# Kernel tuning notes

Measured on AMD Instinct MI355X. Metric: run time of the kernel, lower is better.

## Reference

```python
import jax, jax.numpy as jnp
import numpy as np

N = 4096          # batch size / number of points
D_DATA = 1024     # data feature dim
D_LATENT = 64     # latent dim
REG_LAMBDA = 0.5


def _pdist(x):
    """Pairwise Euclidean distance matrix [N, N] via the gram trick.

    Equivalent to norm(x[None, :, :] - x[:, None, :], axis=-1) but avoids the
    N x N x D intermediate. Safe sqrt so the (zero) diagonal has zero gradient.
    """
    sq = jnp.sum(x * x, axis=-1)                      # [N]
    g = x @ x.T                                       # [N, N] gram
    d2 = jnp.maximum(sq[:, None] + sq[None, :] - 2.0 * g, 0.0)
    pos = d2 > 0
    d = jnp.sqrt(jnp.where(pos, d2, 1.0))
    return jnp.where(pos, d, 0.0)


def _mst_edges(dist):
    """Edges (i, j) of the minimum spanning tree of the complete graph with
    edge weights dist[i, j] (0d persistent homology death edges).
    Prim's algorithm, vectorized per step via lax.scan. Returns [N-1, 2] int32.
    """
    n = dist.shape[0]
    in_tree = jnp.zeros(n, dtype=bool).at[0].set(True)
    min_dist = dist[0]                                # best distance to tree
    min_src = jnp.zeros(n, dtype=jnp.int32)           # tree node achieving it

    def step(carry, _):
        in_tree, min_dist, min_src = carry
        masked = jnp.where(in_tree, jnp.inf, min_dist)
        j = jnp.argmin(masked).astype(jnp.int32)
        edge = jnp.stack([min_src[j], j])
        in_tree = in_tree.at[j].set(True)
        dj = dist[j]
        upd = dj < min_dist
        min_dist = jnp.where(upd, dj, min_dist)
        min_src = jnp.where(upd, j, min_src)
        return (in_tree, min_dist, min_src), edge

    _, edges = jax.lax.scan(step, (in_tree, min_dist, min_src), None, length=n - 1)
    return edges  # [N-1, 2]


def _gather(dist, edges):
    return dist[edges[:, 0], edges[:, 1]]  # [N-1]


def setup_inputs() -> dict:
    key = jax.random.key(0)
    k1, k2, k3 = jax.random.split(key, 3)
    return {
        "y_true": jax.random.normal(k1, (N, D_DATA), dtype=jnp.float32),
        "latent": jax.random.normal(k2, (N, D_LATENT), dtype=jnp.float32),
        "y_pred": jax.random.normal(k3, (N, D_DATA), dtype=jnp.float32),
        "latent_norm": jnp.array(1.0, dtype=jnp.float32),
    }


def reference(y_true, latent, y_pred, latent_norm):
    # keras MSE: mean over last axis -> per-sample vector [N]
    ae_loss = jnp.mean((y_true - y_pred) ** 2, axis=-1)

    data_distances = _pdist(y_true)
    data_distances = data_distances / jnp.max(data_distances)
    latent_distances = _pdist(latent) / latent_norm

    e_data = _mst_edges(jax.lax.stop_gradient(data_distances))
    data_loss = jnp.mean((_gather(data_distances, e_data)
                          - _gather(latent_distances, e_data)) ** 2)

    e_lat = _mst_edges(jax.lax.stop_gradient(latent_distances))
    latent_loss = jnp.mean((_gather(data_distances, e_lat)
                            - _gather(latent_distances, e_lat)) ** 2)

    topo_loss = data_loss + latent_loss
    return ae_loss + REG_LAMBDA * topo_loss  # [N] (scalar topo broadcast)
```

## Files before the change

### kernel.cpp

```cpp
#include <hip/hip_runtime.h>
#include <math.h>

#define N_PTS 4096
#define DD 1024
#define DL 64
#define NEDGE (N_PTS - 1)
#define B_ROUNDS 12
#define NT 32

typedef __attribute__((ext_vector_type(8))) short short8;
typedef __attribute__((ext_vector_type(4))) float floatx4;
typedef __attribute__((ext_vector_type(4))) unsigned short ushortx4;

__device__ __forceinline__ unsigned short f2bf(float f) {
  unsigned u = __float_as_uint(f);
  u = u + 0x7FFFu + ((u >> 16) & 1u);
  return (unsigned short)(u >> 16);
}

__global__ __launch_bounds__(256) void ae_sq_kernel(const float* __restrict__ yt,
                                                    const float* __restrict__ yp,
                                                    float* __restrict__ out,
                                                    float* __restrict__ sqD,
                                                    unsigned short* __restrict__ Xb) {
  int row = blockIdx.x, tid = threadIdx.x;
  const float4* a = (const float4*)(yt + (size_t)row * DD);
  const float4* b = (const float4*)(yp + (size_t)row * DD);
  float4 va = a[tid], vb = b[tid];
  ushortx4 o = {f2bf(va.x), f2bf(va.y), f2bf(va.z), f2bf(va.w)};
  *(ushortx4*)(Xb + (size_t)row * DD + tid * 4) = o;
  float e0 = va.x - vb.x, e1 = va.y - vb.y, e2 = va.z - vb.z, e3 = va.w - vb.w;
  float se = e0 * e0 + e1 * e1 + e2 * e2 + e3 * e3;
  float ss = va.x * va.x + va.y * va.y + va.z * va.z + va.w * va.w;
  for (int off = 32; off > 0; off >>= 1) {
    se += __shfl_down(se, off);
    ss += __shfl_down(ss, off);
  }
  __shared__ float sse[4], sss[4];
  int lane = tid & 63, w = tid >> 6;
  if (lane == 0) { sse[w] = se; sss[w] = ss; }
  __syncthreads();
  if (tid == 0) {
    out[row] = (sse[0] + sse[1] + sse[2] + sse[3]) * (1.0f / DD);
    sqD[row] = sss[0] + sss[1] + sss[2] + sss[3];
  }
}

__global__ __launch_bounds__(256) void sql_kernel(const float* __restrict__ lat,
                                                  float* __restrict__ sqL,
                                                  unsigned short* __restrict__ Lb) {
  int row = blockIdx.x * 4 + (threadIdx.x >> 6);
  int lane = threadIdx.x & 63;
  float v = lat[(size_t)row * DL + lane];
  Lb[(size_t)row * DL + lane] = f2bf(v);
  float s = v * v;
  for (int off = 32; off > 0; off >>= 1) s += __shfl_down(s, off);
  if (lane == 0) sqL[row] = s;
}

__global__ __launch_bounds__(1024) void norm_kernel(const float* __restrict__ sqD,
                                                    const float* __restrict__ sqL,
                                                    unsigned int* __restrict__ normbits) {
  const float* s = blockIdx.x ? sqL : sqD;
  int tid = threadIdx.x;
  float m = fmaxf(fmaxf(s[tid], s[tid + 1024]), fmaxf(s[tid + 2048], s[tid + 3072]));
  for (int off = 32; off > 0; off >>= 1) m = fmaxf(m, __shfl_down(m, off));
  __shared__ float sm[16];
  int lane = tid & 63, w = tid >> 6;
  if (lane == 0) sm[w] = m;
  __syncthreads();
  if (tid == 0) {
    float mm = sm[0];
    for (int k = 1; k < 16; ++k) mm = fmaxf(mm, sm[k]);
    normbits[blockIdx.x] = __float_as_uint(mm);
  }
}

__global__ __launch_bounds__(256) void dist_mfma(const unsigned short* __restrict__ Xb,
                                                 const unsigned short* __restrict__ Lb,
                                                 const float* __restrict__ sqD,
                                                 const float* __restrict__ sqL,
                                                 unsigned short* __restrict__ dD,
                                                 unsigned short* __restrict__ dL,
                                                 const unsigned int* __restrict__ normbits,
                                                 unsigned int* __restrict__ maxbits) {
  int inst = blockIdx.y;
  const unsigned short* X = inst ? Lb : Xb;
  const float* sq = inst ? sqL : sqD;
  unsigned short* dist = inst ? dL : dD;
  int K = inst ? DL : DD;
  float scale = 65535.0f / (2.0f * sqrtf(__uint_as_float(normbits[inst])) + 1e-12f);

  int bi = 0, rem = blockIdx.x, span = NT;
  while (rem >= span) { rem -= span; ++bi; --span; }
  int bj = bi + rem;
  int row0 = bi * 128, col0 = bj * 128;

  __shared__ short As[128 * 40];
  __shared__ short Bs[128 * 40];
  int tid = threadIdx.x;
  int wave = tid >> 6, lane = tid & 63;
  int m = lane & 15, q = lane >> 4;
  int rw = (wave >> 1) * 64, cw = (wave & 1) * 64;

  floatx4 acc[4][4];
#pragma unroll
  for (int mi = 0; mi < 4; ++mi)
#pragma unroll
    for (int ni = 0; ni < 4; ++ni) acc[mi][ni] = {0.f, 0.f, 0.f, 0.f};

  int s0 = tid, s1 = tid + 256;
  int r0 = s0 >> 2, p0 = s0 & 3, r1 = s1 >> 2, p1 = s1 & 3;

  for (int k0 = 0; k0 < K; k0 += 32) {
    short8 a0 = *(const short8*)(X + (size_t)(row0 + r0) * K + k0 + p0 * 8);
    short8 a1 = *(const short8*)(X + (size_t)(row0 + r1) * K + k0 + p1 * 8);
    short8 b0 = *(const short8*)(X + (size_t)(col0 + r0) * K + k0 + p0 * 8);
    short8 b1 = *(const short8*)(X + (size_t)(col0 + r1) * K + k0 + p1 * 8);
    __syncthreads();
    *(short8*)&As[r0 * 40 + p0 * 8] = a0;
    *(short8*)&As[r1 * 40 + p1 * 8] = a1;
    *(short8*)&Bs[r0 * 40 + p0 * 8] = b0;
    *(short8*)&Bs[r1 * 40 + p1 * 8] = b1;
    __syncthreads();
    short8 aF[4], bF[4];
#pragma unroll
    for (int mi = 0; mi < 4; ++mi)
      aF[mi] = *(const short8*)&As[(rw + mi * 16 + m) * 40 + q * 8];
#pragma unroll
    for (int ni = 0; ni < 4; ++ni)
      bF[ni] = *(const short8*)&Bs[(cw + ni * 16 + m) * 40 + q * 8];
#pragma unroll
    for (int mi = 0; mi < 4; ++mi)
#pragma unroll
      for (int ni = 0; ni < 4; ++ni)
        acc[mi][ni] = __builtin_amdgcn_mfma_f32_16x16x32_bf16(aF[mi], bF[ni],
                                                              acc[mi][ni], 0, 0, 0);
  }

  float bmax = 0.f;
#pragma unroll
  for (int mi = 0; mi < 4; ++mi) {
    int i0 = row0 + rw + mi * 16 + q * 4;
    float s_i[4] = {sq[i0], sq[i0 + 1], sq[i0 + 2], sq[i0 + 3]};
#pragma unroll
    for (int ni = 0; ni < 4; ++ni) {
      int j = col0 + cw + ni * 16 + m;
      float sj = sq[j];
      ushortx4 tvec;
#pragma unroll
      for (int r = 0; r < 4; ++r) {
        float d2 = s_i[r] + sj - 2.f * acc[mi][ni][r];
        float d = d2 > 0.f ? sqrtf(d2) : 0.f;
        bmax = fmaxf(bmax, d);
        unsigned short u = (unsigned short)fminf(d * scale, 65535.0f);
        dist[(size_t)(i0 + r) * N_PTS + j] = u;
        tvec[r] = u;
      }
      *(ushortx4*)&dist[(size_t)j * N_PTS + i0] = tvec;
    }
  }
  if (inst == 0) {
    for (int off = 32; off > 0; off >>= 1) bmax = fmaxf(bmax, __shfl_down(bmax, off));
    __shared__ float bm[4];
    if (lane == 0) bm[wave] = bmax;
    __syncthreads();
    if (tid == 0)
      atomicMax(maxbits, __float_as_uint(fmaxf(fmaxf(bm[0], bm[1]), fmaxf(bm[2], bm[3]))));
  }
}

__global__ __launch_bounds__(256) void segmin_kernel(const unsigned short* __restrict__ dD,
                                                     const unsigned short* __restrict__ dL,
                                                     unsigned int* __restrict__ segKey) {
  int inst = blockIdx.y;
  const unsigned short* dist = inst ? dL : dD;
  unsigned int* segK = segKey + (size_t)inst * N_PTS * 64;
  int tid = threadIdx.x, wave = tid >> 6, lane = tid & 63;
  int row = blockIdx.x * 4 + wave;
  const uint4* rowp = (const uint4*)(dist + (size_t)row * N_PTS);
  unsigned mk = 0xFFFFFFFFu;
  int colbase = lane * 64;
#pragma unroll
  for (int t = 0; t < 8; ++t) {
    uint4 v = rowp[lane * 8 + t];
    unsigned e[8] = {v.x & 0xFFFFu, v.x >> 16, v.y & 0xFFFFu, v.y >> 16,
                     v.z & 0xFFFFu, v.z >> 16, v.w & 0xFFFFu, v.w >> 16};
#pragma unroll
    for (int u = 0; u < 8; ++u)
      mk = min(mk, (e[u] << 12) | (unsigned)(colbase + t * 8 + u));
  }
  segK[(size_t)row * 64 + lane] = mk;
}

__global__ __launch_bounds__(256) void boruvka_init(unsigned short* __restrict__ comp,
                                                    unsigned long long* __restrict__ bestKey,
                                                    int* __restrict__ numRoots,
                                                    int* __restrict__ edgeCnt) {
  int i = blockIdx.x * 256 + threadIdx.x;
  if (i < N_PTS) {
    comp[i] = (unsigned short)i;
    comp[N_PTS + i] = (unsigned short)i;
    bestKey[i] = ~0ULL;
    bestKey[N_PTS + i] = ~0ULL;
  }
  if (i == 0) {
    numRoots[0] = N_PTS; numRoots[1] = N_PTS;
    edgeCnt[0] = 0; edgeCnt[1] = 0;
  }
}

__global__ __launch_bounds__(256) void boruvka_scan(const unsigned short* __restrict__ dD,
                                                    const unsigned short* __restrict__ dL,
                                                    const unsigned int* __restrict__ segKey,
                                                    const unsigned short* __restrict__ comp,
                                                    unsigned long long* __restrict__ bestKey,
                                                    const int* __restrict__ numRoots) {
  int inst = blockIdx.y;
  if (numRoots[inst] <= 1) return;
  const unsigned short* dist = inst ? dL : dD;
  const unsigned int* segK = segKey + (size_t)inst * N_PTS * 64;
  const unsigned short* compI = comp + (size_t)inst * N_PTS;
  unsigned long long* bkI = bestKey + (size_t)inst * N_PTS;
  int tid = threadIdx.x, wave = tid >> 6, lane = tid & 63;

  int row = blockIdx.x * 4 + wave;
  unsigned myc = compI[row];
  unsigned skey = segK[(size_t)row * 64 + lane];
#pragma unroll
  for (int k = 2; k <= 64; k <<= 1)
#pragma unroll
    for (int j = k >> 1; j > 0; j >>= 1) {
      unsigned p = __shfl_xor(skey, j);
      unsigned mn = min(skey, p), mx = max(skey, p);
      skey = (((lane & k) == 0) == ((lane & j) == 0)) ? mn : mx;
    }
  unsigned best = 0xFFFFFFFFu;
  const unsigned short* rowp = dist + (size_t)row * N_PTS;
  int i = 0;
  while (i < 64) {
    unsigned k0 = __shfl(skey, i);
    if (k0 >= best) break;
    unsigned k1 = (i < 63) ? __shfl(skey, i + 1) : 0xFFFFFFFFu;
    int b0 = (int)(k0 & 0xFC0u);
    unsigned d0v = rowp[b0 + lane];
    unsigned c0v = compI[b0 + lane];
    unsigned cand = (c0v != myc) ? ((d0v << 12) | (unsigned)(b0 + lane)) : 0xFFFFFFFFu;
    if (k1 < best) {
      int b1 = (int)(k1 & 0xFC0u);
      unsigned d1v = rowp[b1 + lane];
      unsigned c1v = compI[b1 + lane];
      unsigned c2 = (c1v != myc) ? ((d1v << 12) | (unsigned)(b1 + lane)) : 0xFFFFFFFFu;
      cand = min(cand, c2);
    }
#pragma unroll
    for (int off = 32; off > 0; off >>= 1) cand = min(cand, __shfl_xor(cand, off));
    best = min(best, cand);
    i += 2;
  }
  if (lane == 0 && best != 0xFFFFFFFFu) {
    unsigned dd16 = best >> 12;
    int j = (int)(best & 0xFFFu);
    int lo = row < j ? row : j, hi = row < j ? j : row;
    unsigned long long key40 = ((unsigned long long)dd16 << 24) |
                               ((unsigned long long)lo << 12) | (unsigned long long)hi;
    if (key40 < bkI[myc]) atomicMin(&bkI[myc], key40);
  }
}

__global__ __launch_bounds__(1024) void boruvka_merge(unsigned short* __restrict__ comp,
                                                      unsigned long long* __restrict__ bestKey,
                                                      int* __restrict__ numRoots,
                                                      int2* __restrict__ edges,
                                                      int* __restrict__ edgeCnt) {
  int inst = blockIdx.x;
  if (numRoots[inst] <= 1) return;
  unsigned short* compI = comp + (size_t)inst * N_PTS;
  unsigned long long* bkI = bestKey + (size_t)inst * N_PTS;
  edges += (size_t)inst * NEDGE;

  __shared__ unsigned short comp_s[N_PTS];
  __shared__ unsigned short parent_s[N_PTS];
  __shared__ unsigned long long key_s[N_PTS];
  __shared__ int scn[1024];
  __shared__ int rootCnt;
  int tid = threadIdx.x;
  if (tid == 0) rootCnt = 0;
  for (int i = tid; i < N_PTS / 4; i += 1024)
    ((uint2*)comp_s)[i] = ((const uint2*)compI)[i];
  for (int i = tid; i < N_PTS / 2; i += 1024)
    ((uint4*)key_s)[i] = ((const uint4*)bkI)[i];
  __syncthreads();

  int cnt = 0;
  int2 ebuf[4];
#pragma unroll
  for (int k = 0; k < 4; ++k) {
    int c = tid + k * 1024;
    unsigned short p = (unsigned short)c;
    if (comp_s[c] == c) {
      unsigned long long key = key_s[c];
      bkI[c] = ~0ULL;
      if (key != ~0ULL) {
        int lo = (int)((key >> 12) & 0xFFF), hi = (int)(key & 0xFFF);
        int c2 = (comp_s[lo] == c) ? comp_s[hi] : comp_s[lo];
        bool mutual = (key_s[c2] == key);
        bool add;
        if (mutual) {
          if (c < c2) add = true;
          else { p = (unsigned short)c2; add = false; }
        } else { p = (unsigned short)c2; add = true; }
        if (add) ebuf[cnt++] = make_int2(lo, hi);
      }
    }
    parent_s[c] = p;
  }
  scn[tid] = cnt;
  __syncthreads();
  for (int s = 1; s < 1024; s <<= 1) {
    int v = (tid >= s) ? scn[tid - s] : 0;
    __syncthreads();
    scn[tid] += v;
    __syncthreads();
  }
  int base = edgeCnt[inst] + scn[tid] - cnt;
  for (int k = 0; k < cnt; ++k)
    if (base + k < NEDGE) edges[base + k] = ebuf[k];
  if (tid == 1023) edgeCnt[inst] += scn[1023];
  for (int it = 0; it < 12; ++it) {
    __syncthreads();
#pragma unroll
    for (int k = 0; k < 4; ++k) {
      int c = tid + k * 1024;
      parent_s[c] = parent_s[parent_s[c]];
    }
  }
  __syncthreads();
  int local = 0;
#pragma unroll
  for (int k = 0; k < 4; ++k) {
    int c = tid + k * 1024;
    compI[c] = parent_s[comp_s[c]];
    if (comp_s[c] == c && parent_s[c] == c) local++;
  }
  atomicAdd(&rootCnt, local);
  __syncthreads();
  if (tid == 0) numRoots[inst] = rootCnt;
}

__global__ __launch_bounds__(256) void loss_kernel(const unsigned short* __restrict__ dD,
                                                   const unsigned short* __restrict__ dL,
                                                   const int2* __restrict__ edges_all,
                                                   const unsigned int* __restrict__ maxbits,
                                                   const unsigned int* __restrict__ normbits,
                                                   const float* __restrict__ latent_norm,
                                                   float* __restrict__ sums) {
  int tid = threadIdx.x;
  int e = blockIdx.x * 256 + tid;
  float facD = (2.0f * sqrtf(__uint_as_float(normbits[0])) + 1e-12f) * (1.0f / 65535.0f) /
               __uint_as_float(*maxbits);
  float facL = (2.0f * sqrtf(__uint_as_float(normbits[1])) + 1e-12f) * (1.0f / 65535.0f) /
               latent_norm[0];
  float v0 = 0.f, v1 = 0.f;
  if (e < 2 * NEDGE) {
    int2 ed = edges_all[e];
    int i = ed.x & (N_PTS - 1), j = ed.y & (N_PTS - 1);
    float dd = (float)dD[(size_t)i * N_PTS + j] * facD;
    float ld = (float)dL[(size_t)i * N_PTS + j] * facL;
    float df = dd - ld;
    if (e < NEDGE) v0 = df * df; else v1 = df * df;
  }
  for (int off = 32; off > 0; off >>= 1) {
    v0 += __shfl_down(v0, off);
    v1 += __shfl_down(v1, off);
  }
  __shared__ float s0[4], s1[4];
  int lane = tid & 63, w = tid >> 6;
  if (lane == 0) { s0[w] = v0; s1[w] = v1; }
  __syncthreads();
  if (tid == 0) {
    float t0 = s0[0] + s0[1] + s0[2] + s0[3];
    float t1 = s1[0] + s1[1] + s1[2] + s1[3];
    if (t0 != 0.f) atomicAdd(&sums[0], t0);
    if (t1 != 0.f) atomicAdd(&sums[1], t1);
  }
}

__global__ __launch_bounds__(256) void finalize_kernel(float* __restrict__ out,
                                                       const float* __restrict__ sums) {
  int i = blockIdx.x * blockDim.x + threadIdx.x;
  float topo = (sums[0] + sums[1]) * (1.0f / NEDGE);
  out[i] += 0.5f * topo;
}

extern "C" void kernel_launch(void* const* d_in, const int* in_sizes, int n_in,
                              void* d_out, int out_size, void* d_ws, size_t ws_size,
                              hipStream_t stream) {
  const float* y_true = (const float*)d_in[0];
  const float* latent = (const float*)d_in[1];
  const float* y_pred = (const float*)d_in[2];
  const float* latent_norm = (const float*)d_in[3];
  float* out = (float*)d_out;
  char* ws = (char*)d_ws;

  const size_t MAT16 = (size_t)N_PTS * N_PTS * 2;
  size_t off = 0;
  unsigned short* dD = (unsigned short*)(ws + off); off += MAT16;
  unsigned short* dL = (unsigned short*)(ws + off); off += MAT16;
  unsigned short* Xb = (unsigned short*)(ws + off); off += (size_t)N_PTS * DD * 2;
  unsigned short* Lb = (unsigned short*)(ws + off); off += (size_t)N_PTS * DL * 2;
  float* sqD = (float*)(ws + off); off += (size_t)N_PTS * 4;
  float* sqL = (float*)(ws + off); off += (size_t)N_PTS * 4;
  int2* edges = (int2*)(ws + off); off += (size_t)2 * NEDGE * 8 + 16;
  unsigned long long* bestKey = (unsigned long long*)(ws + off); off += (size_t)2 * N_PTS * 8;
  unsigned short* comp = (unsigned short*)(ws + off); off += (size_t)2 * N_PTS * 2;
  unsigned int* segKey = (unsigned int*)(ws + off); off += (size_t)2 * N_PTS * 64 * 4;
  int* numRoots = (int*)(ws + off); off += 256;
  int* edgeCnt = numRoots + 2;
  unsigned int* maxbits = (unsigned int*)(edgeCnt + 2);
  float* sums = (float*)(maxbits + 1);
  unsigned int* normbits = (unsigned int*)(sums + 2);

  hipMemsetAsync(numRoots, 0, 256, stream);

  ae_sq_kernel<<<N_PTS, 256, 0, stream>>>(y_true, y_pred, out, sqD, Xb);
  sql_kernel<<<N_PTS / 4, 256, 0, stream>>>(latent, sqL, Lb);
  norm_kernel<<<2, 1024, 0, stream>>>(sqD, sqL, normbits);
  boruvka_init<<<N_PTS / 256, 256, 0, stream>>>(comp, bestKey, numRoots, edgeCnt);

  int tri = NT * (NT + 1) / 2;
  dist_mfma<<<dim3(tri, 2), 256, 0, stream>>>(Xb, Lb, sqD, sqL, dD, dL, normbits, maxbits);
  segmin_kernel<<<dim3(N_PTS / 4, 2), 256, 0, stream>>>(dD, dL, segKey);

  for (int r = 0; r < B_ROUNDS; ++r) {
    boruvka_scan<<<dim3(N_PTS / 4, 2), 256, 0, stream>>>(dD, dL, segKey, comp, bestKey,
                                                         numRoots);
    boruvka_merge<<<2, 1024, 0, stream>>>(comp, bestKey, numRoots, edges, edgeCnt);
  }

  loss_kernel<<<32, 256, 0, stream>>>(dD, dL, edges, maxbits, normbits, latent_norm, sums);
  finalize_kernel<<<N_PTS / 256, 256, 0, stream>>>(out, sums);
}
```

Before: 288.6 us.

## Fuse segment-min into distance GEMM and merge Boruvka scan/merge into one kernel

Segment minima are now computed in the dist_mfma epilogue with shuffles and atomicMin, so the separate segmin pass that re-read both 32 MB distance matrices is gone. Each Boruvka round becomes a single kernel. Every block redundantly performs the previous round's merge in shared memory: it loads comp and bestKey, does pointer jumping, and only block 0 writes edges and comp. Then it runs the scan. Double-buffered comp/bestKey with round tags avoid resetting keys between rounds, but every one of the 2048 blocks now repeats the merge work.

```diff
diff --git a/kernel.cpp b/kernel.cpp
--- a/kernel.cpp
+++ b/kernel.cpp
@@ -76,18 +76,38 @@
   }
 }
 
+__global__ __launch_bounds__(256) void boruvka_init(unsigned short* __restrict__ compP0,
+                                                    unsigned long long* __restrict__ bk,
+                                                    unsigned int* __restrict__ segKey,
+                                                    int* __restrict__ numRoots,
+                                                    int* __restrict__ edgeCnt) {
+  int i = blockIdx.x * 256 + threadIdx.x;
+  if (i < 2 * N_PTS * 64) segKey[i] = 0xFFFFFFFFu;
+  if (i < 2 * 2 * N_PTS) bk[i] = ~0ULL;
+  if (i < N_PTS) {
+    compP0[i] = (unsigned short)i;
+    compP0[N_PTS + i] = (unsigned short)i;
+  }
+  if (i == 0) {
+    numRoots[0] = N_PTS; numRoots[1] = N_PTS;
+    edgeCnt[0] = 0; edgeCnt[1] = 0;
+  }
+}
+
 __global__ __launch_bounds__(256) void dist_mfma(const unsigned short* __restrict__ Xb,
                                                  const unsigned short* __restrict__ Lb,
                                                  const float* __restrict__ sqD,
                                                  const float* __restrict__ sqL,
                                                  unsigned short* __restrict__ dD,
                                                  unsigned short* __restrict__ dL,
+                                                 unsigned int* __restrict__ segKey,
                                                  const unsigned int* __restrict__ normbits,
                                                  unsigned int* __restrict__ maxbits) {
   int inst = blockIdx.y;
   const unsigned short* X = inst ? Lb : Xb;
   const float* sq = inst ? sqL : sqD;
   unsigned short* dist = inst ? dL : dD;
+  unsigned int* segK = segKey + (size_t)inst * N_PTS * 64;
   int K = inst ? DL : DD;
   float scale = 65535.0f / (2.0f * sqrtf(__uint_as_float(normbits[inst])) + 1e-12f);
 
@@ -138,11 +158,14 @@
                                                               acc[mi][ni], 0, 0, 0);
   }
 
+  int segU = (col0 + cw) >> 6, segL = (row0 + rw) >> 6;
   float bmax = 0.f;
+  unsigned ml[4] = {~0u, ~0u, ~0u, ~0u};
 #pragma unroll
   for (int mi = 0; mi < 4; ++mi) {
     int i0 = row0 + rw + mi * 16 + q * 4;
     float s_i[4] = {sq[i0], sq[i0 + 1], sq[i0 + 2], sq[i0 + 3]};
+    unsigned mu[4] = {~0u, ~0u, ~0u, ~0u};
 #pragma unroll
     for (int ni = 0; ni < 4; ++ni) {
       int j = col0 + cw + ni * 16 + m;
@@ -153,13 +176,28 @@
         float d2 = s_i[r] + sj - 2.f * acc[mi][ni][r];
         float d = d2 > 0.f ? sqrtf(d2) : 0.f;
         bmax = fmaxf(bmax, d);
-        unsigned short u = (unsigned short)fminf(d * scale, 65535.0f);
-        dist[(size_t)(i0 + r) * N_PTS + j] = u;
-        tvec[r] = u;
+        unsigned u = (unsigned)fminf(d * scale, 65535.0f);
+        dist[(size_t)(i0 + r) * N_PTS + j] = (unsigned short)u;
+        tvec[r] = (unsigned short)u;
+        mu[r] = min(mu[r], (u << 12) | (unsigned)j);
+        ml[ni] = min(ml[ni], (u << 12) | (unsigned)(i0 + r));
       }
       *(ushortx4*)&dist[(size_t)j * N_PTS + i0] = tvec;
     }
-  }
+#pragma unroll
+    for (int r = 0; r < 4; ++r) {
+      unsigned v = mu[r];
+      v = min(v, __shfl_xor(v, 1));
+      v = min(v, __shfl_xor(v, 2));
+      v = min(v, __shfl_xor(v, 4));
+      v = min(v, __shfl_xor(v, 8));
+      if (m == 0) atomicMin(&segK[(size_t)(i0 + r) * 64 + segU], v);
+    }
+  }
+#pragma unroll
+  for (int ni = 0; ni < 4; ++ni)
+    atomicMin(&segK[(size_t)(col0 + cw + ni * 16 + m) * 64 + segL], ml[ni]);
+
   if (inst == 0) {
     for (int off = 32; off > 0; off >>= 1) bmax = fmaxf(bmax, __shfl_down(bmax, off));
     __shared__ float bm[4];
@@ -170,62 +208,105 @@
   }
 }
 
-__global__ __launch_bounds__(256) void segmin_kernel(const unsigned short* __restrict__ dD,
+__global__ __launch_bounds__(256) void boruvka_round(const unsigned short* __restrict__ dD,
                                                      const unsigned short* __restrict__ dL,
-                                                     unsigned int* __restrict__ segKey) {
-  int inst = blockIdx.y;
-  const unsigned short* dist = inst ? dL : dD;
-  unsigned int* segK = segKey + (size_t)inst * N_PTS * 64;
-  int tid = threadIdx.x, wave = tid >> 6, lane = tid & 63;
-  int row = blockIdx.x * 4 + wave;
-  const uint4* rowp = (const uint4*)(dist + (size_t)row * N_PTS);
-  unsigned mk = 0xFFFFFFFFu;
-  int colbase = lane * 64;
-#pragma unroll
-  for (int t = 0; t < 8; ++t) {
-    uint4 v = rowp[lane * 8 + t];
-    unsigned e[8] = {v.x & 0xFFFFu, v.x >> 16, v.y & 0xFFFFu, v.y >> 16,
-                     v.z & 0xFFFFu, v.z >> 16, v.w & 0xFFFFu, v.w >> 16};
-#pragma unroll
-    for (int u = 0; u < 8; ++u)
-      mk = min(mk, (e[u] << 12) | (unsigned)(colbase + t * 8 + u));
-  }
-  segK[(size_t)row * 64 + lane] = mk;
-}
-
-__global__ __launch_bounds__(256) void boruvka_init(unsigned short* __restrict__ comp,
-                                                    unsigned long long* __restrict__ bestKey,
-                                                    int* __restrict__ numRoots,
-                                                    int* __restrict__ edgeCnt) {
-  int i = blockIdx.x * 256 + threadIdx.x;
-  if (i < N_PTS) {
-    comp[i] = (unsigned short)i;
-    comp[N_PTS + i] = (unsigned short)i;
-    bestKey[i] = ~0ULL;
-    bestKey[N_PTS + i] = ~0ULL;
-  }
-  if (i == 0) {
-    numRoots[0] = N_PTS; numRoots[1] = N_PTS;
-    edgeCnt[0] = 0; edgeCnt[1] = 0;
-  }
-}
-
-__global__ __launch_bounds__(256) void boruvka_scan(const unsigned short* __restrict__ dD,
-                                                    const unsigned short* __restrict__ dL,
-                                                    const unsigned int* __restrict__ segKey,
-                                                    const unsigned short* __restrict__ comp,
-                                                    unsigned long long* __restrict__ bestKey,
-                                                    const int* __restrict__ numRoots) {
+                                                     const unsigned int* __restrict__ segKey,
+                                                     const unsigned short* __restrict__ compIn,
+                                                     unsigned short* __restrict__ compOut,
+                                                     const unsigned long long* __restrict__ bkRead,
+                                                     unsigned long long* __restrict__ bkWrite,
+                                                     int tagR,
+                                                     int* __restrict__ numRoots,
+                                                     int2* __restrict__ edges,
+                                                     int* __restrict__ edgeCnt) {
   int inst = blockIdx.y;
   if (numRoots[inst] <= 1) return;
   const unsigned short* dist = inst ? dL : dD;
   const unsigned int* segK = segKey + (size_t)inst * N_PTS * 64;
-  const unsigned short* compI = comp + (size_t)inst * N_PTS;
-  unsigned long long* bkI = bestKey + (size_t)inst * N_PTS;
+  const unsigned short* cin = compIn + (size_t)inst * N_PTS;
+  unsigned short* cout = compOut + (size_t)inst * N_PTS;
+  const unsigned long long* bkr = bkRead + (size_t)inst * N_PTS;
+  unsigned long long* bkw = bkWrite + (size_t)inst * N_PTS;
+
+  __shared__ __align__(16) unsigned short comp_s[N_PTS];
+  __shared__ __align__(16) unsigned short parent_s[N_PTS];
+  __shared__ __align__(16) unsigned long long key_s[N_PTS];
+  __shared__ int scn[256];
+  __shared__ int rootCnt;
   int tid = threadIdx.x, wave = tid >> 6, lane = tid & 63;
+  unsigned long long vtag = (unsigned long long)(tagR + 1);
+
+  if (tid == 0) rootCnt = 0;
+  for (int i = tid; i < N_PTS / 8; i += 256)
+    ((uint4*)comp_s)[i] = ((const uint4*)cin)[i];
+  for (int i = tid; i < N_PTS / 2; i += 256)
+    ((uint4*)key_s)[i] = ((const uint4*)bkr)[i];
+  __syncthreads();
+
+  int cnt = 0;
+  for (int c = tid; c < N_PTS; c += 256) {
+    unsigned short p = (unsigned short)c;
+    if (comp_s[c] == c) {
+      unsigned long long key = key_s[c];
+      if ((key >> 40) == vtag) {
+        int lo = (int)((key >> 12) & 0xFFF), hi = (int)(key & 0xFFF);
+        int c2 = (comp_s[lo] == c) ? comp_s[hi] : comp_s[lo];
+        bool mutual = (key_s[c2] == key);
+        if (mutual) {
+          if (c < c2) cnt++;
+          else p = (unsigned short)c2;
+        } else { p = (unsigned short)c2; cnt++; }
+      }
+    }
+    parent_s[c] = p;
+  }
+  __syncthreads();
+  if (blockIdx.x == 0) {
+    scn[tid] = cnt;
+    __syncthreads();
+    for (int s = 1; s < 256; s <<= 1) {
+      int v = (tid >= s) ? scn[tid - s] : 0;
+      __syncthreads();
+      scn[tid] += v;
+      __syncthreads();
+    }
+    int base = edgeCnt[inst] + scn[tid] - cnt;
+    for (int c = tid; c < N_PTS; c += 256) {
+      if (comp_s[c] == c) {
+        unsigned long long key = key_s[c];
+        if ((key >> 40) == vtag) {
+          int lo = (int)((key >> 12) & 0xFFF), hi = (int)(key & 0xFFF);
+          int c2 = (comp_s[lo] == c) ? comp_s[hi] : comp_s[lo];
+          bool mutual = (key_s[c2] == key);
+          if (!mutual || c < c2)
+            if (base < NEDGE) edges[(size_t)inst * NEDGE + base++] = make_int2(lo, hi);
+        }
+      }
+    }
+    if (tid == 255) edgeCnt[inst] += scn[255];
+  }
+  for (int it = 0; it < 12; ++it) {
+    __syncthreads();
+    for (int c = tid; c < N_PTS; c += 256) parent_s[c] = parent_s[parent_s[c]];
+  }
+  __syncthreads();
+  int local = 0;
+  for (int c = tid; c < N_PTS; c += 256) {
+    unsigned short old = comp_s[c];
+    if (old == c && parent_s[c] == c) local++;
+    comp_s[c] = parent_s[old];
+  }
+  atomicAdd(&rootCnt, local);
+  __syncthreads();
+  if (blockIdx.x == 0) {
+    for (int i = tid; i < N_PTS / 8; i += 256)
+      ((uint4*)cout)[i] = ((const uint4*)comp_s)[i];
+    if (tid == 0) numRoots[inst] = rootCnt;
+  }
+  if (rootCnt <= 1) return;
 
   int row = blockIdx.x * 4 + wave;
-  unsigned myc = compI[row];
+  unsigned myc = comp_s[row];
   unsigned skey = segK[(size_t)row * 64 + lane];
 #pragma unroll
   for (int k = 2; k <= 64; k <<= 1)
@@ -244,12 +325,12 @@
     unsigned k1 = (i < 63) ? __shfl(skey, i + 1) : 0xFFFFFFFFu;
     int b0 = (int)(k0 & 0xFC0u);
     unsigned d0v = rowp[b0 + lane];
-    unsigned c0v = compI[b0 + lane];
+    unsigned c0v = comp_s[b0 + lane];
     unsigned cand = (c0v != myc) ? ((d0v << 12) | (unsigned)(b0 + lane)) : 0xFFFFFFFFu;
     if (k1 < best) {
       int b1 = (int)(k1 & 0xFC0u);
       unsigned d1v = rowp[b1 + lane];
-      unsigned c1v = compI[b1 + lane];
+      unsigned c1v = comp_s[b1 + lane];
       unsigned c2 = (c1v != myc) ? ((d1v << 12) | (unsigned)(b1 + lane)) : 0xFFFFFFFFu;
       cand = min(cand, c2);
     }
@@ -262,90 +343,11 @@
     unsigned dd16 = best >> 12;
     int j = (int)(best & 0xFFFu);
     int lo = row < j ? row : j, hi = row < j ? j : row;
-    unsigned long long key40 = ((unsigned long long)dd16 << 24) |
-                               ((unsigned long long)lo << 12) | (unsigned long long)hi;
-    if (key40 < bkI[myc]) atomicMin(&bkI[myc], key40);
-  }
-}
-
-__global__ __launch_bounds__(1024) void boruvka_merge(unsigned short* __restrict__ comp,
-                                                      unsigned long long* __restrict__ bestKey,
-                                                      int* __restrict__ numRoots,
-                                                      int2* __restrict__ edges,
-                                                      int* __restrict__ edgeCnt) {
-  int inst = blockIdx.x;
-  if (numRoots[inst] <= 1) return;
-  unsigned short* compI = comp + (size_t)inst * N_PTS;
-  unsigned long long* bkI = bestKey + (size_t)inst * N_PTS;
-  edges += (size_t)inst * NEDGE;
-
-  __shared__ unsigned short comp_s[N_PTS];
-  __shared__ unsigned short parent_s[N_PTS];
-  __shared__ unsigned long long key_s[N_PTS];
-  __shared__ int scn[1024];
-  __shared__ int rootCnt;
-  int tid = threadIdx.x;
-  if (tid == 0) rootCnt = 0;
-  for (int i = tid; i < N_PTS / 4; i += 1024)
-    ((uint2*)comp_s)[i] = ((const uint2*)compI)[i];
-  for (int i = tid; i < N_PTS / 2; i += 1024)
-    ((uint4*)key_s)[i] = ((const uint4*)bkI)[i];
-  __syncthreads();
-
-  int cnt = 0;
-  int2 ebuf[4];
-#pragma unroll
-  for (int k = 0; k < 4; ++k) {
-    int c = tid + k * 1024;
-    unsigned short p = (unsigned short)c;
-    if (comp_s[c] == c) {
-      unsigned long long key = key_s[c];
-      bkI[c] = ~0ULL;
-      if (key != ~0ULL) {
-        int lo = (int)((key >> 12) & 0xFFF), hi = (int)(key & 0xFFF);
-        int c2 = (comp_s[lo] == c) ? comp_s[hi] : comp_s[lo];
-        bool mutual = (key_s[c2] == key);
-        bool add;
-        if (mutual) {
-          if (c < c2) add = true;
-          else { p = (unsigned short)c2; add = false; }
-        } else { p = (unsigned short)c2; add = true; }
-        if (add) ebuf[cnt++] = make_int2(lo, hi);
-      }
-    }
-    parent_s[c] = p;
-  }
-  scn[tid] = cnt;
-  __syncthreads();
-  for (int s = 1; s < 1024; s <<= 1) {
-    int v = (tid >= s) ? scn[tid - s] : 0;
-    __syncthreads();
-    scn[tid] += v;
-    __syncthreads();
-  }
-  int base = edgeCnt[inst] + scn[tid] - cnt;
-  for (int k = 0; k < cnt; ++k)
-    if (base + k < NEDGE) edges[base + k] = ebuf[k];
-  if (tid == 1023) edgeCnt[inst] += scn[1023];
-  for (int it = 0; it < 12; ++it) {
-    __syncthreads();
-#pragma unroll
-    for (int k = 0; k < 4; ++k) {
-      int c = tid + k * 1024;
-      parent_s[c] = parent_s[parent_s[c]];
-    }
-  }
-  __syncthreads();
-  int local = 0;
-#pragma unroll
-  for (int k = 0; k < 4; ++k) {
-    int c = tid + k * 1024;
-    compI[c] = parent_s[comp_s[c]];
-    if (comp_s[c] == c && parent_s[c] == c) local++;
-  }
-  atomicAdd(&rootCnt, local);
-  __syncthreads();
-  if (tid == 0) numRoots[inst] = rootCnt;
+    unsigned long long key = ((unsigned long long)tagR << 40) |
+                             ((unsigned long long)dd16 << 24) |
+                             ((unsigned long long)lo << 12) | (unsigned long long)hi;
+    if (key < bkw[myc]) atomicMin(&bkw[myc], key);
+  }
 }
 
 __global__ __launch_bounds__(256) void loss_kernel(const unsigned short* __restrict__ dD,
@@ -412,8 +414,8 @@
   float* sqD = (float*)(ws + off); off += (size_t)N_PTS * 4;
   float* sqL = (float*)(ws + off); off += (size_t)N_PTS * 4;
   int2* edges = (int2*)(ws + off); off += (size_t)2 * NEDGE * 8 + 16;
-  unsigned long long* bestKey = (unsigned long long*)(ws + off); off += (size_t)2 * N_PTS * 8;
-  unsigned short* comp = (unsigned short*)(ws + off); off += (size_t)2 * N_PTS * 2;
+  unsigned long long* bk = (unsigned long long*)(ws + off); off += (size_t)2 * 2 * N_PTS * 8;
+  unsigned short* compP = (unsigned short*)(ws + off); off += (size_t)2 * 2 * N_PTS * 2;
   unsigned int* segKey = (unsigned int*)(ws + off); off += (size_t)2 * N_PTS * 64 * 4;
   int* numRoots = (int*)(ws + off); off += 256;
   int* edgeCnt = numRoots + 2;
@@ -426,16 +428,22 @@
   ae_sq_kernel<<<N_PTS, 256, 0, stream>>>(y_true, y_pred, out, sqD, Xb);
   sql_kernel<<<N_PTS / 4, 256, 0, stream>>>(latent, sqL, Lb);
   norm_kernel<<<2, 1024, 0, stream>>>(sqD, sqL, normbits);
-  boruvka_init<<<N_PTS / 256, 256, 0, stream>>>(comp, bestKey, numRoots, edgeCnt);
+  boruvka_init<<<(2 * N_PTS * 64 + 255) / 256, 256, 0, stream>>>(compP, bk, segKey,
+                                                                 numRoots, edgeCnt);
 
   int tri = NT * (NT + 1) / 2;
-  dist_mfma<<<dim3(tri, 2), 256, 0, stream>>>(Xb, Lb, sqD, sqL, dD, dL, normbits, maxbits);
-  segmin_kernel<<<dim3(N_PTS / 4, 2), 256, 0, stream>>>(dD, dL, segKey);
-
-  for (int r = 0; r < B_ROUNDS; ++r) {
-    boruvka_scan<<<dim3(N_PTS / 4, 2), 256, 0, stream>>>(dD, dL, segKey, comp, bestKey,
-                                                         numRoots);
-    boruvka_merge<<<2, 1024, 0, stream>>>(comp, bestKey, numRoots, edges, edgeCnt);
+  dist_mfma<<<dim3(tri, 2), 256, 0, stream>>>(Xb, Lb, sqD, sqL, dD, dL, segKey,
+                                              normbits, maxbits);
+
+  for (int r = 0; r <= B_ROUNDS; ++r) {
+    unsigned short* cin = compP + (size_t)(r & 1) * 2 * N_PTS;
+    unsigned short* cout = compP + (size_t)((r + 1) & 1) * 2 * N_PTS;
+    unsigned long long* bkr = bk + (size_t)((r + 1) & 1) * 2 * N_PTS;
+    unsigned long long* bkw = bk + (size_t)(r & 1) * 2 * N_PTS;
+    int tagR = B_ROUNDS + 1 - r;
+    boruvka_round<<<dim3(N_PTS / 4, 2), 256, 0, stream>>>(dD, dL, segKey, cin, cout, bkr,
+                                                          bkw, tagR, numRoots, edges,
+                                                          edgeCnt);
   }
 
   loss_kernel<<<32, 256, 0, stream>>>(dD, dL, edges, maxbits, normbits, latent_norm, sums);
```

Result: slower. 614.0 us (+112.8%).
